# Performance work log

Hardware: AMD Instinct MI355X
Metric: run time of the kernel (lower is better)

## Reference

```python
import jax, jax.numpy as jnp
import numpy as np

SUB_NO = 20
T_NO = 201
E_NO = 2000
I_NO = 500
T_DATA = 20000

def _make_cden():
    C = np.zeros((SUB_NO, SUB_NO), dtype=np.float32)
    for i in range(SUB_NO):
        for c in (2 * i + 1, 2 * i + 2):
            if c < SUB_NO:
                C[i, c] = 1.0
    return C

C_DEN = _make_cden()
CHILDREN = [np.where(C_DEN[s] == 1)[0] for s in range(SUB_NO)]  # static tree structure


def setup_inputs() -> dict:
    key = jax.random.key(0)
    ks = jax.random.split(key, 12)
    eps = 1e-6
    inp = {}
    inp['S_e'] = jax.random.uniform(ks[0], (T_DATA, E_NO), dtype=jnp.float32)
    inp['S_i'] = jax.random.uniform(ks[1], (T_DATA, I_NO), dtype=jnp.float32)
    # uniform noise for REBAR reparam; clipped away from {0,1} so log(-log(u)) is finite
    inp['u'] = jnp.clip(jax.random.uniform(ks[2], (SUB_NO, E_NO + I_NO), dtype=jnp.float32), eps, 1.0 - eps)
    inp['v'] = jnp.clip(jax.random.uniform(ks[3], (SUB_NO, E_NO + I_NO), dtype=jnp.float32), eps, 1.0 - eps)
    inp['W_syn'] = jax.random.normal(ks[4], (SUB_NO, 2), dtype=jnp.float32) * 0.1
    inp['Tau_syn'] = jnp.ones((SUB_NO, 2), dtype=jnp.float32)
    inp['Delta_syn'] = jax.random.uniform(ks[5], (SUB_NO, 2), dtype=jnp.float32)
    inp['W_sub'] = jax.random.uniform(ks[6], (SUB_NO,), dtype=jnp.float32)
    inp['V_o'] = jax.random.normal(ks[7], (1,), dtype=jnp.float32)
    inp['Theta'] = jnp.zeros((SUB_NO,), dtype=jnp.float32)
    inp['C_syn_log'] = jnp.ones((SUB_NO, E_NO + I_NO), dtype=jnp.float32)
    return inp


def _H(x):
    # one-hot of per-column argmax (first max, as torch.argmax)
    idx = jnp.argmax(x, axis=0)
    return jax.nn.one_hot(idx, x.shape[0], axis=0, dtype=x.dtype)


def _reparam_pz(u, theta):
    return jnp.log(theta) - jnp.log(-jnp.log(u))


def _reparam_pz_b(v, b, theta):
    # b is one-hot per column; v_k = v at the b==1 row of each column
    v_k = jnp.sum(v * b, axis=0, keepdims=True)  # [1, cols]
    z_same = -jnp.log(-jnp.log(v))
    z_diff = -jnp.log(-jnp.log(v) / theta - jnp.log(v_k))
    return b * z_same + (1.0 - b) * z_diff


def _evaluate_f(C_syn, S_e, S_i, W_syn, Tau_syn, Delta_syn, W_sub, V_o):
    T_data = S_e.shape[0]
    C_syn_e = C_syn[:, :E_NO]          # [sub, E]
    C_syn_i = C_syn[:, -I_NO:]         # [sub, I]
    # double-exponential (alpha) synaptic kernels, vectorized over subunits & e/i
    t_raw = jnp.arange(T_NO, dtype=S_e.dtype)                               # [T_no]
    t = jnp.maximum(t_raw[None, None, :] - jnp.exp(Delta_syn)[:, :, None], 0.0)  # [sub,2,T_no]
    t_tau = t / jnp.exp(Tau_syn)[:, :, None]
    kern = t_tau * jnp.exp(-t_tau) * W_syn[:, :, None]                      # [sub,2,T_no]
    # project spikes onto subunits
    in_e = S_e @ C_syn_e.T   # [T, sub]
    in_i = S_i @ C_syn_i.T   # [T, sub]
    # causal depthwise conv: syn[t,s] = sum_tau kern[s,:,tau] * in[t-tau,s]
    inp = jnp.stack([in_e.T, in_i.T], axis=1).reshape(1, SUB_NO * 2, T_data)   # NCH
    k = jnp.flip(kern, axis=-1).reshape(SUB_NO * 2, 1, T_NO)                   # OIH
    filt = jax.lax.conv_general_dilated(
        inp, k, window_strides=(1,), padding=[(T_NO - 1, 0)],
        feature_group_count=SUB_NO * 2,
        dimension_numbers=('NCH', 'OIH', 'NCH'))
    syn_in = filt.reshape(SUB_NO, 2, T_data).sum(axis=1).T   # [T, sub]
    # tree-recurrent tanh aggregation (children have higher index than parents)
    sub_out = [None] * SUB_NO
    for s in range(SUB_NO):
        idx = SUB_NO - 1 - s
        ch = CHILDREN[idx]
        if ch.size == 0:
            sub_out[idx] = jnp.tanh(syn_in[:, idx])
        else:
            leaf = sum(sub_out[c] * W_sub[c] for c in ch)
            sub_out[idx] = jnp.tanh(syn_in[:, idx] + leaf)
    return sub_out[0] * W_sub[0] + V_o[0]


def reference(S_e, S_i, u, v, W_syn, Tau_syn, Delta_syn, W_sub, V_o, Theta, C_syn_log):
    theta = jax.nn.softmax(C_syn_log, axis=0)
    rebar_z = _reparam_pz(u, theta)
    hard_z = _H(rebar_z)
    rebar_zb = _reparam_pz_b(v, hard_z, theta)
    soft_z = jax.nn.sigmoid(rebar_z / 0.5) + 1e-9
    soft_zb = jax.nn.sigmoid(rebar_zb / 0.5) + 1e-9
    V_hard_z = _evaluate_f(hard_z, S_e, S_i, W_syn, Tau_syn, Delta_syn, W_sub, V_o)
    V_soft_z = _evaluate_f(soft_z, S_e, S_i, W_syn, Tau_syn, Delta_syn, W_sub, V_o)
    V_soft_zb = _evaluate_f(soft_zb, S_e, S_i, W_syn, Tau_syn, Delta_syn, W_sub, V_o)
    return (V_hard_z, V_soft_z, V_soft_zb, theta, hard_z, soft_z, soft_zb)
```

## Files before the change

### kernel.cpp

```cpp
#include <hip/hip_runtime.h>
#include <math.h>

#define SUBS 20
#define TAPS 201
#define ENO 2000
#define INO 500
#define TDATA 20000

typedef __bf16 bf16x8 __attribute__((ext_vector_type(8)));
typedef float f32x4 __attribute__((ext_vector_type(4)));

#define WGE_STRIDE 2048
#define WGI_STRIDE 512

#define WGE_OFF  0ull
#define WGI_OFF  262144ull
#define KERN_OFF 327680ull
#define INE_OFF  360448ull
#define INI_OFF  (INE_OFF + 4800000ull)
#define P1_OFF   (INI_OFF + 4800000ull)
#define P2_OFF   (P1_OFF  + 4800000ull)
#define P3_OFF   (P2_OFF  + 4800000ull)
#define SYN_OFF  (P3_OFF  + 4800000ull)

__device__ __forceinline__ unsigned short f2bf(float f) {
  union { float f; unsigned int u; } c; c.f = f;
  unsigned int u = c.u;
  return (unsigned short)((u + 0x7FFFu + ((u >> 16) & 1u)) >> 16);
}

__device__ __forceinline__ float fast_tanh(float x) {
  const float ax = fabsf(x);
  const float e  = __expf(2.f * ax);
  const float t  = 1.f - 2.f / (e + 1.f);
  return copysignf(t, x);
}

__global__ __launch_bounds__(256) void prep_kernel(
    const float* __restrict__ u, const float* __restrict__ v,
    const float* __restrict__ C_log, const float* __restrict__ W_syn,
    const float* __restrict__ Tau_syn, const float* __restrict__ Delta_syn,
    float* __restrict__ out,
    unsigned short* __restrict__ wge, unsigned short* __restrict__ wgi,
    float* __restrict__ kern)
{
  if (blockIdx.x < 10) {
    const int n = blockIdx.x * 256 + threadIdx.x;
    if (n >= 2500) return;
    float x[SUBS], theta[SUBS], rebar[SUBS];
    float mx = -1e30f;
#pragma unroll
    for (int s = 0; s < SUBS; ++s) { x[s] = C_log[s*2500 + n]; mx = fmaxf(mx, x[s]); }
    float sum = 0.f;
#pragma unroll
    for (int s = 0; s < SUBS; ++s) { theta[s] = __expf(x[s] - mx); sum += theta[s]; }
    const float inv = 1.f / sum;
    int idx = 0; float best = -1e30f;
#pragma unroll
    for (int s = 0; s < SUBS; ++s) {
      theta[s] *= inv;
      out[60000 + s*2500 + n] = theta[s];
      const float uu = u[s*2500 + n];
      const float r = __logf(theta[s]) - __logf(-__logf(uu));
      rebar[s] = r;
      if (r > best) { best = r; idx = s; }
    }
    const float lvk = __logf(v[idx*2500 + n]);
#pragma unroll
    for (int s = 0; s < SUBS; ++s) {
      const float hz = (s == idx) ? 1.f : 0.f;
      const float sz = 1.f / (1.f + __expf(-2.f * rebar[s])) + 1e-9f;
      const float vv = v[s*2500 + n];
      const float zb = (s == idx) ? (-__logf(-__logf(vv)))
                                  : (-__logf(-__logf(vv) / theta[s] - lvk));
      const float szb = 1.f / (1.f + __expf(-2.f * zb)) + 1e-9f;
      out[110000 + s*2500 + n] = hz;
      out[160000 + s*2500 + n] = sz;
      out[210000 + s*2500 + n] = szb;
      if (n < ENO) {
        wge[(s     )*WGE_STRIDE + n] = f2bf(hz);
        wge[(20 + s)*WGE_STRIDE + n] = f2bf(sz);
        wge[(40 + s)*WGE_STRIDE + n] = f2bf(szb);
      } else {
        const int k = n - ENO;
        wgi[(s     )*WGI_STRIDE + k] = f2bf(hz);
        wgi[(20 + s)*WGI_STRIDE + k] = f2bf(sz);
        wgi[(40 + s)*WGI_STRIDE + k] = f2bf(szb);
      }
    }
  } else {
    const int tid = threadIdx.x;
    for (int i = tid; i < 40*TAPS; i += 256) {
      const int ch = i / TAPS, m = i - ch*TAPS;
      const float dl  = __expf(Delta_syn[ch]);
      const float tau = __expf(Tau_syn[ch]);
      const float t  = fmaxf((float)m - dl, 0.f);
      const float tt = t / tau;
      kern[i] = tt * __expf(-tt) * W_syn[ch];
    }
    for (int i = tid; i < 4*2048; i += 256) wge[(60 + (i >> 11))*WGE_STRIDE + (i & 2047)] = 0;
    for (int i = tid; i < 60*48;  i += 256) wge[(i / 48)*WGE_STRIDE + 2000 + (i % 48)] = 0;
    for (int i = tid; i < 4*512;  i += 256) wgi[(60 + (i >> 9))*WGI_STRIDE + (i & 511)] = 0;
    for (int i = tid; i < 60*12;  i += 256) wgi[(i / 12)*WGI_STRIDE + 500 + (i % 12)] = 0;
  }
}

__global__ __launch_bounds__(512) void gemm_kernel(
    const float* __restrict__ S_e, const float* __restrict__ S_i,
    const unsigned short* __restrict__ wge, const unsigned short* __restrict__ wgi,
    float* __restrict__ in_e, float* __restrict__ in_i,
    float* __restrict__ P1, float* __restrict__ P2, float* __restrict__ P3)
{
  __shared__ unsigned short Alds[128*72];
  __shared__ unsigned short Blds[64*72];
  const int tid  = threadIdx.x;
  const int wave = tid >> 6;
  const int lane = tid & 63;
  const int m16  = lane & 15;
  const int quad = lane >> 4;
  const int t0   = blockIdx.x * 128;
  const int cy   = blockIdx.y;
  const bool isE = (cy < 4);

  const float* S = isE ? S_e : S_i;
  const unsigned short* Wg = isE ? wge : wgi;
  float* outp = (cy == 0) ? in_e : (cy == 1) ? P1 : (cy == 2) ? P2
              : (cy == 3) ? P3   : in_i;
  const int K       = isE ? ENO : INO;
  const int Wstride = isE ? WGE_STRIDE : WGI_STRIDE;
  const int k_base  = isE ? cy * 512 : 0;
  const int steps   = 8;

  const int rowA  = tid >> 2;
  const int slotA = tid & 3;
  const int rowB  = tid >> 3;
  const int slotB = tid & 7;
  const int tA    = t0 + rowA;
  const float* Arow = S + (size_t)((tA < TDATA) ? tA : TDATA - 1) * K;
  const unsigned short* Brow = Wg + (size_t)rowB * Wstride;

  f32x4 acc0 = {0.f,0.f,0.f,0.f};
  f32x4 acc1 = acc0, acc2 = acc0, acc3 = acc0;

  for (int st = 0; st < steps; ++st) {
    const int k0 = k_base + st * 64;
    const uint4 bw = *(const uint4*)(Brow + k0 + slotB*8);
    float4 v0, v1, v2, v3;
    {
      const int kb = k0 + slotA*16;
      const int c0 = (kb +  4 <= K) ? kb      : K - 4;
      const int c1 = (kb +  8 <= K) ? kb +  4 : K - 4;
      const int c2 = (kb + 12 <= K) ? kb +  8 : K - 4;
      const int c3 = (kb + 16 <= K) ? kb + 12 : K - 4;
      v0 = *(const float4*)(Arow + c0);
      v1 = *(const float4*)(Arow + c1);
      v2 = *(const float4*)(Arow + c2);
      v3 = *(const float4*)(Arow + c3);
    }
    ushort4 p0, p1, p2, p3;
    p0.x = f2bf(v0.x); p0.y = f2bf(v0.y); p0.z = f2bf(v0.z); p0.w = f2bf(v0.w);
    p1.x = f2bf(v1.x); p1.y = f2bf(v1.y); p1.z = f2bf(v1.z); p1.w = f2bf(v1.w);
    p2.x = f2bf(v2.x); p2.y = f2bf(v2.y); p2.z = f2bf(v2.z); p2.w = f2bf(v2.w);
    p3.x = f2bf(v3.x); p3.y = f2bf(v3.y); p3.z = f2bf(v3.z); p3.w = f2bf(v3.w);
    unsigned short* adst = &Alds[rowA*72 + slotA*16];
    *(ushort4*)(adst    ) = p0;  *(ushort4*)(adst + 4) = p1;
    *(ushort4*)(adst + 8) = p2;  *(ushort4*)(adst +12) = p3;
    *(uint4*)(&Blds[rowB*72 + slotB*8]) = bw;
    __syncthreads();
#pragma unroll
    for (int h = 0; h < 2; ++h) {
      const int kh = h*32 + quad*8;
      const bf16x8 a  = *(const bf16x8*)(&Alds[(wave*16 + m16)*72 + kh]);
      const bf16x8 b0 = *(const bf16x8*)(&Blds[(      m16)*72 + kh]);
      const bf16x8 b1 = *(const bf16x8*)(&Blds[(16 + m16)*72 + kh]);
      const bf16x8 b2 = *(const bf16x8*)(&Blds[(32 + m16)*72 + kh]);
      const bf16x8 b3 = *(const bf16x8*)(&Blds[(48 + m16)*72 + kh]);
      acc0 = __builtin_amdgcn_mfma_f32_16x16x32_bf16(a, b0, acc0, 0, 0, 0);
      acc1 = __builtin_amdgcn_mfma_f32_16x16x32_bf16(a, b1, acc1, 0, 0, 0);
      acc2 = __builtin_amdgcn_mfma_f32_16x16x32_bf16(a, b2, acc2, 0, 0, 0);
      acc3 = __builtin_amdgcn_mfma_f32_16x16x32_bf16(a, b3, acc3, 0, 0, 0);
    }
    __syncthreads();
  }
  const int t = t0 + wave*16 + quad*4;
  if (t < TDATA) {
    float* o = outp + t;
    *(float4*)(o + (size_t)(     m16)*TDATA) = *(float4*)&acc0;
    *(float4*)(o + (size_t)(16 + m16)*TDATA) = *(float4*)&acc1;
    *(float4*)(o + (size_t)(32 + m16)*TDATA) = *(float4*)&acc2;
    if (m16 < 12)
      *(float4*)(o + (size_t)(48 + m16)*TDATA) = *(float4*)&acc3;
  }
}

__device__ __forceinline__ int swz(int i) { return i + (i >> 5); }

__global__ __launch_bounds__(256) void conv_kernel(
    const float* __restrict__ in_e, const float* __restrict__ P1,
    const float* __restrict__ P2,  const float* __restrict__ P3,
    const float* __restrict__ in_i,
    const float* __restrict__ kern, float* __restrict__ syn)
{
  __shared__ float Ee[2320];
  __shared__ float Ei[2320];
  const int ch = blockIdx.y;
  const int t0 = blockIdx.x * 2048;
  const int s  = ch % SUBS;
  const size_t off = (size_t)ch * TDATA;
  for (int i = threadIdx.x; i < 2248; i += 256) {
    const int g = t0 - 200 + i;
    float e = 0.f, ii = 0.f;
    if (g >= 0 && g < TDATA) {
      e = in_e[off + g] + P1[off + g] + P2[off + g] + P3[off + g];
      ii = in_i[off + g];
    }
    Ee[swz(i)] = e;
    Ei[swz(i)] = ii;
  }
  __syncthreads();
  const float* ke = kern + (size_t)(s*2    ) * TAPS;
  const float* ki = kern + (size_t)(s*2 + 1) * TAPS;
  const int tb = threadIdx.x * 8;
  float acc[8] = {0.f,0.f,0.f,0.f,0.f,0.f,0.f,0.f};
  float we[8], wi[8];
#pragma unroll
  for (int j = 0; j < 8; ++j) {
    we[j] = Ee[swz(tb + 200 + j)];
    wi[j] = Ei[swz(tb + 200 + j)];
  }
#pragma unroll 8
  for (int m = 0; m < TAPS; ++m) {
    const float k0 = ke[m];
    const float k1 = ki[m];
#pragma unroll
    for (int j = 0; j < 8; ++j)
      acc[j] = fmaf(we[j], k0, fmaf(wi[j], k1, acc[j]));
    if (m < TAPS - 1) {
#pragma unroll
      for (int j = 7; j > 0; --j) { we[j] = we[j-1]; wi[j] = wi[j-1]; }
      we[0] = Ee[swz(tb + 199 - m)];
      wi[0] = Ei[swz(tb + 199 - m)];
    }
  }
  const int t = t0 + tb;
  if (t < TDATA) {
    float* o = syn + off + t;
    *(float4*)(o    ) = make_float4(acc[0], acc[1], acc[2], acc[3]);
    *(float4*)(o + 4) = make_float4(acc[4], acc[5], acc[6], acc[7]);
  }
}

__global__ __launch_bounds__(256) void tree_kernel(
    const float* __restrict__ syn, const float* __restrict__ W_sub,
    const float* __restrict__ V_o, float* __restrict__ out)
{
  const int t = blockIdx.x * 256 + threadIdx.x;
  const int var = blockIdx.y;
  if (t >= TDATA) return;
  const float* sp = syn + (size_t)var * SUBS * TDATA + t;
  float so[SUBS];
#pragma unroll
  for (int s = SUBS - 1; s >= 0; --s) {
    float val = sp[(size_t)s * TDATA];
    const int c1 = 2*s + 1, c2 = 2*s + 2;
    if (c1 < SUBS) val += so[c1] * W_sub[c1];
    if (c2 < SUBS) val += so[c2] * W_sub[c2];
    so[s] = fast_tanh(val);
  }
  out[(size_t)var * TDATA + t] = so[0] * W_sub[0] + V_o[0];
}

extern "C" void kernel_launch(void* const* d_in, const int* in_sizes, int n_in,
                              void* d_out, int out_size, void* d_ws, size_t ws_size,
                              hipStream_t stream) {
  const float* S_e     = (const float*)d_in[0];
  const float* S_i     = (const float*)d_in[1];
  const float* u       = (const float*)d_in[2];
  const float* v       = (const float*)d_in[3];
  const float* W_syn   = (const float*)d_in[4];
  const float* Tau_syn = (const float*)d_in[5];
  const float* Delta   = (const float*)d_in[6];
  const float* W_sub   = (const float*)d_in[7];
  const float* V_o     = (const float*)d_in[8];
  const float* C_log   = (const float*)d_in[10];
  float* out = (float*)d_out;
  char* ws = (char*)d_ws;
  unsigned short* wge = (unsigned short*)(ws + WGE_OFF);
  unsigned short* wgi = (unsigned short*)(ws + WGI_OFF);
  float* kern = (float*)(ws + KERN_OFF);
  float* in_e = (float*)(ws + INE_OFF);
  float* in_i = (float*)(ws + INI_OFF);
  float* P1   = (float*)(ws + P1_OFF);
  float* P2   = (float*)(ws + P2_OFF);
  float* P3   = (float*)(ws + P3_OFF);
  float* syn  = (float*)(ws + SYN_OFF);

  prep_kernel<<<dim3(11), dim3(256), 0, stream>>>(u, v, C_log, W_syn, Tau_syn,
                                                  Delta, out, wge, wgi, kern);
  gemm_kernel<<<dim3(157, 5), dim3(512), 0, stream>>>(
      S_e, S_i, wge, wgi, in_e, in_i, P1, P2, P3);
  conv_kernel<<<dim3(10, 60), dim3(256), 0, stream>>>(in_e, P1, P2, P3, in_i,
                                                      kern, syn);
  tree_kernel<<<dim3(79, 3), dim3(256), 0, stream>>>(syn, W_sub, V_o, out);
}
```

Measured before the change: 337.0 us.

## Prefetch next GEMM k-tile into registers and halve block tile to 64 rows

The GEMM kernel now loads the next 64-wide k-slice of A and B into registers while the current slice is converted and multiplied, giving register double-buffering that hides global-load latency. The block is shrunk from 128 to 64 time rows with 256 threads, doubling the grid to 313x5 so more blocks spread across CUs. This adds register pressure and B-tile reloads per block, and each thread now also loads two B vectors.

```diff
diff --git a/kernel.cpp b/kernel.cpp
--- a/kernel.cpp
+++ b/kernel.cpp
@@ -105,20 +105,32 @@
   }
 }
 
-__global__ __launch_bounds__(512) void gemm_kernel(
+#define LOAD_A(k0, d0, d1, d2, d3) do {                          \
+    const int kb_ = (k0) + slotA*16;                             \
+    const int c0_ = (kb_ +  4 <= K) ? kb_      : K - 4;          \
+    const int c1_ = (kb_ +  8 <= K) ? kb_ +  4 : K - 4;          \
+    const int c2_ = (kb_ + 12 <= K) ? kb_ +  8 : K - 4;          \
+    const int c3_ = (kb_ + 16 <= K) ? kb_ + 12 : K - 4;          \
+    d0 = *(const float4*)(Arow + c0_);                           \
+    d1 = *(const float4*)(Arow + c1_);                           \
+    d2 = *(const float4*)(Arow + c2_);                           \
+    d3 = *(const float4*)(Arow + c3_);                           \
+  } while (0)
+
+__global__ __launch_bounds__(256) void gemm_kernel(
     const float* __restrict__ S_e, const float* __restrict__ S_i,
     const unsigned short* __restrict__ wge, const unsigned short* __restrict__ wgi,
     float* __restrict__ in_e, float* __restrict__ in_i,
     float* __restrict__ P1, float* __restrict__ P2, float* __restrict__ P3)
 {
-  __shared__ unsigned short Alds[128*72];
+  __shared__ unsigned short Alds[64*72];
   __shared__ unsigned short Blds[64*72];
   const int tid  = threadIdx.x;
   const int wave = tid >> 6;
   const int lane = tid & 63;
   const int m16  = lane & 15;
   const int quad = lane >> 4;
-  const int t0   = blockIdx.x * 128;
+  const int t0   = blockIdx.x * 64;
   const int cy   = blockIdx.y;
   const bool isE = (cy < 4);
 
@@ -129,43 +141,44 @@
   const int K       = isE ? ENO : INO;
   const int Wstride = isE ? WGE_STRIDE : WGI_STRIDE;
   const int k_base  = isE ? cy * 512 : 0;
-  const int steps   = 8;
 
   const int rowA  = tid >> 2;
   const int slotA = tid & 3;
-  const int rowB  = tid >> 3;
-  const int slotB = tid & 7;
   const int tA    = t0 + rowA;
   const float* Arow = S + (size_t)((tA < TDATA) ? tA : TDATA - 1) * K;
-  const unsigned short* Brow = Wg + (size_t)rowB * Wstride;
+  const unsigned short* Brow = Wg + (size_t)rowA * Wstride + slotA*16;
 
   f32x4 acc0 = {0.f,0.f,0.f,0.f};
   f32x4 acc1 = acc0, acc2 = acc0, acc3 = acc0;
 
-  for (int st = 0; st < steps; ++st) {
-    const int k0 = k_base + st * 64;
-    const uint4 bw = *(const uint4*)(Brow + k0 + slotB*8);
-    float4 v0, v1, v2, v3;
-    {
-      const int kb = k0 + slotA*16;
-      const int c0 = (kb +  4 <= K) ? kb      : K - 4;
-      const int c1 = (kb +  8 <= K) ? kb +  4 : K - 4;
-      const int c2 = (kb + 12 <= K) ? kb +  8 : K - 4;
-      const int c3 = (kb + 16 <= K) ? kb + 12 : K - 4;
-      v0 = *(const float4*)(Arow + c0);
-      v1 = *(const float4*)(Arow + c1);
-      v2 = *(const float4*)(Arow + c2);
-      v3 = *(const float4*)(Arow + c3);
+  float4 a0, a1, a2, a3, n0, n1, n2, n3;
+  uint4 bw0, bw1, nb0, nb1;
+  {
+    const int k0 = k_base;
+    bw0 = *(const uint4*)(Brow + k0);
+    bw1 = *(const uint4*)(Brow + k0 + 8);
+    LOAD_A(k0, a0, a1, a2, a3);
+  }
+
+#pragma unroll
+  for (int st = 0; st < 8; ++st) {
+    if (st < 7) {
+      const int kn = k_base + (st + 1) * 64;
+      nb0 = *(const uint4*)(Brow + kn);
+      nb1 = *(const uint4*)(Brow + kn + 8);
+      LOAD_A(kn, n0, n1, n2, n3);
     }
     ushort4 p0, p1, p2, p3;
-    p0.x = f2bf(v0.x); p0.y = f2bf(v0.y); p0.z = f2bf(v0.z); p0.w = f2bf(v0.w);
-    p1.x = f2bf(v1.x); p1.y = f2bf(v1.y); p1.z = f2bf(v1.z); p1.w = f2bf(v1.w);
-    p2.x = f2bf(v2.x); p2.y = f2bf(v2.y); p2.z = f2bf(v2.z); p2.w = f2bf(v2.w);
-    p3.x = f2bf(v3.x); p3.y = f2bf(v3.y); p3.z = f2bf(v3.z); p3.w = f2bf(v3.w);
+    p0.x = f2bf(a0.x); p0.y = f2bf(a0.y); p0.z = f2bf(a0.z); p0.w = f2bf(a0.w);
+    p1.x = f2bf(a1.x); p1.y = f2bf(a1.y); p1.z = f2bf(a1.z); p1.w = f2bf(a1.w);
+    p2.x = f2bf(a2.x); p2.y = f2bf(a2.y); p2.z = f2bf(a2.z); p2.w = f2bf(a2.w);
+    p3.x = f2bf(a3.x); p3.y = f2bf(a3.y); p3.z = f2bf(a3.z); p3.w = f2bf(a3.w);
     unsigned short* adst = &Alds[rowA*72 + slotA*16];
     *(ushort4*)(adst    ) = p0;  *(ushort4*)(adst + 4) = p1;
     *(ushort4*)(adst + 8) = p2;  *(ushort4*)(adst +12) = p3;
-    *(uint4*)(&Blds[rowB*72 + slotB*8]) = bw;
+    unsigned short* bdst = &Blds[rowA*72 + slotA*16];
+    *(uint4*)(bdst    ) = bw0;
+    *(uint4*)(bdst + 8) = bw1;
     __syncthreads();
 #pragma unroll
     for (int h = 0; h < 2; ++h) {
@@ -181,6 +194,8 @@
       acc3 = __builtin_amdgcn_mfma_f32_16x16x32_bf16(a, b3, acc3, 0, 0, 0);
     }
     __syncthreads();
+    a0 = n0; a1 = n1; a2 = n2; a3 = n3;
+    bw0 = nb0; bw1 = nb1;
   }
   const int t = t0 + wave*16 + quad*4;
   if (t < TDATA) {
@@ -297,7 +312,7 @@
 
   prep_kernel<<<dim3(11), dim3(256), 0, stream>>>(u, v, C_log, W_syn, Tau_syn,
                                                   Delta, out, wge, wgi, kern);
-  gemm_kernel<<<dim3(157, 5), dim3(512), 0, stream>>>(
+  gemm_kernel<<<dim3(313, 5), dim3(256), 0, stream>>>(
       S_e, S_i, wge, wgi, in_e, in_i, P1, P2, P3);
   conv_kernel<<<dim3(10, 60), dim3(256), 0, stream>>>(in_e, P1, P2, P3, in_i,
                                                       kern, syn);
```

Result: no change. 332.0 us (-1.5%).

## Load GEMM operands directly from global into MFMA registers, dropping LDS staging

Applied to the files above, without the earlier changes.

The GEMM kernel no longer stages the A (spike) and B (weight) tiles through shared memory with barriers. Each lane now loads its float4 A fragments and bf16 B fragments straight from global memory, converts A to bf16 in registers, and issues the MFMAs. Block size drops from 512 to 256 threads (64 time rows per block) and the grid doubles. This removes LDS traffic and __syncthreads stalls, but the A loads are strided per row and less coalesced, and B is re-read from global/L2 by every wave.

```diff
diff --git a/kernel.cpp b/kernel.cpp
--- a/kernel.cpp
+++ b/kernel.cpp
@@ -105,20 +105,18 @@
   }
 }
 
-__global__ __launch_bounds__(512) void gemm_kernel(
+__global__ __launch_bounds__(256) void gemm_kernel(
     const float* __restrict__ S_e, const float* __restrict__ S_i,
     const unsigned short* __restrict__ wge, const unsigned short* __restrict__ wgi,
     float* __restrict__ in_e, float* __restrict__ in_i,
     float* __restrict__ P1, float* __restrict__ P2, float* __restrict__ P3)
 {
-  __shared__ unsigned short Alds[128*72];
-  __shared__ unsigned short Blds[64*72];
   const int tid  = threadIdx.x;
   const int wave = tid >> 6;
   const int lane = tid & 63;
   const int m16  = lane & 15;
   const int quad = lane >> 4;
-  const int t0   = blockIdx.x * 128;
+  const int t0   = blockIdx.x * 64;
   const int cy   = blockIdx.y;
   const bool isE = (cy < 4);
 
@@ -129,59 +127,42 @@
   const int K       = isE ? ENO : INO;
   const int Wstride = isE ? WGE_STRIDE : WGI_STRIDE;
   const int k_base  = isE ? cy * 512 : 0;
-  const int steps   = 8;
-
-  const int rowA  = tid >> 2;
-  const int slotA = tid & 3;
-  const int rowB  = tid >> 3;
-  const int slotB = tid & 7;
-  const int tA    = t0 + rowA;
+
+  const int tA = t0 + wave*16 + m16;
   const float* Arow = S + (size_t)((tA < TDATA) ? tA : TDATA - 1) * K;
-  const unsigned short* Brow = Wg + (size_t)rowB * Wstride;
+  const unsigned short* B0 = Wg + (size_t)(m16     ) * Wstride;
+  const unsigned short* B1 = Wg + (size_t)(m16 + 16) * Wstride;
+  const unsigned short* B2 = Wg + (size_t)(m16 + 32) * Wstride;
+  const unsigned short* B3 = Wg + (size_t)(m16 + 48) * Wstride;
 
   f32x4 acc0 = {0.f,0.f,0.f,0.f};
   f32x4 acc1 = acc0, acc2 = acc0, acc3 = acc0;
 
-  for (int st = 0; st < steps; ++st) {
-    const int k0 = k_base + st * 64;
-    const uint4 bw = *(const uint4*)(Brow + k0 + slotB*8);
-    float4 v0, v1, v2, v3;
-    {
-      const int kb = k0 + slotA*16;
-      const int c0 = (kb +  4 <= K) ? kb      : K - 4;
-      const int c1 = (kb +  8 <= K) ? kb +  4 : K - 4;
-      const int c2 = (kb + 12 <= K) ? kb +  8 : K - 4;
-      const int c3 = (kb + 16 <= K) ? kb + 12 : K - 4;
-      v0 = *(const float4*)(Arow + c0);
-      v1 = *(const float4*)(Arow + c1);
-      v2 = *(const float4*)(Arow + c2);
-      v3 = *(const float4*)(Arow + c3);
-    }
-    ushort4 p0, p1, p2, p3;
-    p0.x = f2bf(v0.x); p0.y = f2bf(v0.y); p0.z = f2bf(v0.z); p0.w = f2bf(v0.w);
-    p1.x = f2bf(v1.x); p1.y = f2bf(v1.y); p1.z = f2bf(v1.z); p1.w = f2bf(v1.w);
-    p2.x = f2bf(v2.x); p2.y = f2bf(v2.y); p2.z = f2bf(v2.z); p2.w = f2bf(v2.w);
-    p3.x = f2bf(v3.x); p3.y = f2bf(v3.y); p3.z = f2bf(v3.z); p3.w = f2bf(v3.w);
-    unsigned short* adst = &Alds[rowA*72 + slotA*16];
-    *(ushort4*)(adst    ) = p0;  *(ushort4*)(adst + 4) = p1;
-    *(ushort4*)(adst + 8) = p2;  *(ushort4*)(adst +12) = p3;
-    *(uint4*)(&Blds[rowB*72 + slotB*8]) = bw;
-    __syncthreads();
+#pragma unroll
+  for (int st = 0; st < 8; ++st) {
 #pragma unroll
     for (int h = 0; h < 2; ++h) {
-      const int kh = h*32 + quad*8;
-      const bf16x8 a  = *(const bf16x8*)(&Alds[(wave*16 + m16)*72 + kh]);
-      const bf16x8 b0 = *(const bf16x8*)(&Blds[(      m16)*72 + kh]);
-      const bf16x8 b1 = *(const bf16x8*)(&Blds[(16 + m16)*72 + kh]);
-      const bf16x8 b2 = *(const bf16x8*)(&Blds[(32 + m16)*72 + kh]);
-      const bf16x8 b3 = *(const bf16x8*)(&Blds[(48 + m16)*72 + kh]);
+      const int kh = k_base + st*64 + h*32 + quad*8;
+      const int c0 = (kh + 4 <= K) ? kh     : K - 4;
+      const int c1 = (kh + 8 <= K) ? kh + 4 : K - 4;
+      const float4 va = *(const float4*)(Arow + c0);
+      const float4 vb = *(const float4*)(Arow + c1);
+      const bf16x8 b0 = *(const bf16x8*)(B0 + kh);
+      const bf16x8 b1 = *(const bf16x8*)(B1 + kh);
+      const bf16x8 b2 = *(const bf16x8*)(B2 + kh);
+      const bf16x8 b3 = *(const bf16x8*)(B3 + kh);
+      bf16x8 a;
+      a[0] = (__bf16)va.x; a[1] = (__bf16)va.y;
+      a[2] = (__bf16)va.z; a[3] = (__bf16)va.w;
+      a[4] = (__bf16)vb.x; a[5] = (__bf16)vb.y;
+      a[6] = (__bf16)vb.z; a[7] = (__bf16)vb.w;
       acc0 = __builtin_amdgcn_mfma_f32_16x16x32_bf16(a, b0, acc0, 0, 0, 0);
       acc1 = __builtin_amdgcn_mfma_f32_16x16x32_bf16(a, b1, acc1, 0, 0, 0);
       acc2 = __builtin_amdgcn_mfma_f32_16x16x32_bf16(a, b2, acc2, 0, 0, 0);
       acc3 = __builtin_amdgcn_mfma_f32_16x16x32_bf16(a, b3, acc3, 0, 0, 0);
     }
-    __syncthreads();
-  }
+  }
+
   const int t = t0 + wave*16 + quad*4;
   if (t < TDATA) {
     float* o = outp + t;
@@ -297,7 +278,7 @@
 
   prep_kernel<<<dim3(11), dim3(256), 0, stream>>>(u, v, C_log, W_syn, Tau_syn,
                                                   Delta, out, wge, wgi, kern);
-  gemm_kernel<<<dim3(157, 5), dim3(512), 0, stream>>>(
+  gemm_kernel<<<dim3(313, 5), dim3(256), 0, stream>>>(
       S_e, S_i, wge, wgi, in_e, in_i, P1, P2, P3);
   conv_kernel<<<dim3(10, 60), dim3(256), 0, stream>>>(in_e, P1, P2, P3, in_i,
                                                       kern, syn);
```

After: 346.6 us. +2.9%, slower.
